# Performance work log

Hardware: AMD Instinct MI355X
Metric: run time of the kernel (lower is better)

Reference implementation:

```python
import jax, jax.numpy as jnp
import numpy as np

N_EMBD = 1024
N_HEAD = 16
B, T = 4, 2048


def setup_inputs() -> dict:
    key = jax.random.key(0)
    ks = jax.random.split(key, 4)
    s = 1.0 / np.sqrt(N_EMBD)
    return {
        "x": jax.random.normal(ks[0], (B, T, N_EMBD), dtype=jnp.float32),
        "w_attn": jax.random.normal(ks[1], (N_EMBD, 3 * N_EMBD), dtype=jnp.float32) * s,
        "b_attn": jnp.zeros((3 * N_EMBD,), dtype=jnp.float32),
        "w_proj": jax.random.normal(ks[2], (N_EMBD, N_EMBD), dtype=jnp.float32) * s,
        "b_proj": jnp.zeros((N_EMBD,), dtype=jnp.float32),
    }


def reference(x, w_attn, b_attn, w_proj, b_proj):
    Bb, Tt, C = x.shape
    H = N_HEAD
    D = C // H  # head dim
    qkv = x @ w_attn + b_attn  # [B,T,3C]
    q, k, v = jnp.split(qkv, 3, axis=2)
    # [B,H,T,D]
    q = q.reshape(Bb, Tt, H, D).transpose(0, 2, 1, 3)
    k = k.reshape(Bb, Tt, H, D).transpose(0, 2, 1, 3)
    v = v.reshape(Bb, Tt, H, D).transpose(0, 2, 1, 3)
    scale = 1.0 / np.sqrt(D).astype(np.float32)
    attn = jnp.einsum("bhqd,bhkd->bhqk", q, k) * scale
    mask = jnp.tril(jnp.ones((Tt, Tt), dtype=bool))
    attn = jnp.where(mask, attn, jnp.float32(-jnp.inf))
    probs = jax.nn.softmax(attn, axis=-1)
    out = jnp.einsum("bhqk,bhkd->bhqd", probs, v)
    out = out.transpose(0, 2, 1, 3).reshape(Bb, Tt, C)
    return out @ w_proj + b_proj
```

## Files before the change

### kernel.cpp

```cpp
#include <hip/hip_runtime.h>
#include <hip/hip_bf16.h>


typedef float f32x4 __attribute__((ext_vector_type(4)));
typedef float f32x16 __attribute__((ext_vector_type(16)));
typedef short short8 __attribute__((ext_vector_type(8)));
typedef short short4v __attribute__((ext_vector_type(4)));

__device__ __forceinline__ short f2bf(float f) {
  union { __hip_bfloat16 h; short s; } u;
  u.h = __float2bfloat16(f);
  return u.s;
}

__device__ __forceinline__ void gl_lds16(const void* g, void* l) {
  __builtin_amdgcn_global_load_lds(
      (const __attribute__((address_space(1))) void*)g,
      (__attribute__((address_space(3))) void*)l, 16, 0, 0);
}

__global__ void prep(const float* __restrict__ x, const float* __restrict__ wa,
                     const float* __restrict__ wp, short* __restrict__ xb,
                     short* __restrict__ wat, short* __restrict__ wpt) {
  const int bid = blockIdx.x, tid = threadIdx.x;
  if (bid < 8192) {
    int i = (bid * 256 + tid) * 4;
    float4 v = *(const float4*)(x + i);
    short4v o;
    o[0] = f2bf(v.x); o[1] = f2bf(v.y); o[2] = f2bf(v.z); o[3] = f2bf(v.w);
    *(short4v*)(xb + i) = o;
    return;
  }
  __shared__ float tile[32][33];
  const float* in;
  short* out;
  int N, bx, by;
  if (bid < 11264) {
    int t = bid - 8192;
    in = wa; out = wat; N = 3072; bx = t % 96; by = t / 96;
  } else {
    int t = bid - 11264;
    in = wp; out = wpt; N = 1024; bx = t & 31; by = t >> 5;
  }
  int tx = tid & 31, ty = tid >> 5;
  int x0 = bx * 32, y0 = by * 32;
#pragma unroll
  for (int i = 0; i < 32; i += 8)
    tile[ty + i][tx] = in[(size_t)(y0 + ty + i) * N + x0 + tx];
  __syncthreads();
#pragma unroll
  for (int i = 0; i < 32; i += 8)
    out[(size_t)(x0 + ty + i) * 1024 + y0 + tx] = f2bf(tile[tx][ty + i]);
}

#define GEMM_BODY(A_, Bt_)                                                        \
  __shared__ __align__(16) short As[2][128 * 32];                                 \
  __shared__ __align__(16) short Bs[2][128 * 32];                                 \
  const int tid = threadIdx.x;                                                    \
  const int wv = tid >> 6;                                                        \
  const int wr = wv >> 1, wc = wv & 1;                                            \
  const int col = tid & 31, khalf = (tid >> 5) & 1;                               \
  const int m0 = blockIdx.y * 128, n0 = blockIdx.x * 128;                         \
  const int cc0 = tid, cc1 = tid + 256;                                           \
  const int row0 = cc0 >> 2, part0 = ((cc0 & 3) - ((cc0 >> 3) & 3)) & 3;          \
  const int row1 = cc1 >> 2, part1 = ((cc1 & 3) - ((cc1 >> 3) & 3)) & 3;          \
  const size_t ga0 = (size_t)(m0 + row0) * 1024 + part0 * 8;                      \
  const size_t ga1 = (size_t)(m0 + row1) * 1024 + part1 * 8;                      \
  const size_t gb0 = (size_t)(n0 + row0) * 1024 + part0 * 8;                      \
  const size_t gb1 = (size_t)(n0 + row1) * 1024 + part1 * 8;                      \
  f32x16 acc[2][2];                                                               \
  _Pragma("unroll") for (int i = 0; i < 2; ++i)                                   \
      _Pragma("unroll") for (int j = 0; j < 2; ++j)                               \
          acc[i][j] = (f32x16)(0.f);                                              \
  gl_lds16(A_ + ga0, (char*)As[0] + cc0 * 16);                                    \
  gl_lds16(A_ + ga1, (char*)As[0] + cc1 * 16);                                    \
  gl_lds16(Bt_ + gb0, (char*)Bs[0] + cc0 * 16);                                   \
  gl_lds16(Bt_ + gb1, (char*)Bs[0] + cc1 * 16);                                   \
  __syncthreads();                                                                \
  for (int kt = 0; kt < 32; ++kt) {                                               \
    if (kt + 1 < 32) {                                                            \
      const int k0 = (kt + 1) * 32;                                               \
      char* Ad = (char*)As[(kt + 1) & 1];                                         \
      char* Bd = (char*)Bs[(kt + 1) & 1];                                         \
      gl_lds16(A_ + ga0 + k0, Ad + cc0 * 16);                                     \
      gl_lds16(A_ + ga1 + k0, Ad + cc1 * 16);                                     \
      gl_lds16(Bt_ + gb0 + k0, Bd + cc0 * 16);                                    \
      gl_lds16(Bt_ + gb1 + k0, Bd + cc1 * 16);                                    \
    }                                                                             \
    const short* Ac = As[kt & 1];                                                 \
    const short* Bc = Bs[kt & 1];                                                 \
    short8 af[2][2], bf[2][2];                                                    \
    _Pragma("unroll") for (int i = 0; i < 2; ++i)                                 \
        _Pragma("unroll") for (int s = 0; s < 2; ++s) {                           \
          int pa = s * 2 + khalf;                                                 \
          int ra = wr * 64 + i * 32 + col;                                        \
          int rb = wc * 64 + i * 32 + col;                                        \
          af[i][s] = *(const short8*)&Ac[(ra * 4 + ((pa + (ra >> 1)) & 3)) * 8];  \
          bf[i][s] = *(const short8*)&Bc[(rb * 4 + ((pa + (rb >> 1)) & 3)) * 8];  \
        }                                                                         \
    _Pragma("unroll") for (int s = 0; s < 2; ++s)                                 \
        _Pragma("unroll") for (int i = 0; i < 2; ++i)                             \
            _Pragma("unroll") for (int j = 0; j < 2; ++j)                         \
                acc[i][j] = __builtin_amdgcn_mfma_f32_32x32x16_bf16(              \
                    af[i][s], bf[j][s], acc[i][j], 0, 0, 0);                      \
    __syncthreads();                                                              \
  }

__global__ __launch_bounds__(256, 2) void gemm_qkv(
    const short* __restrict__ A, const short* __restrict__ Bt,
    const float* __restrict__ bias, short* __restrict__ Qb,
    short* __restrict__ Kb, short* __restrict__ Vtb) {
  GEMM_BODY(A, Bt)
  const int rhalf = khalf * 4;
#pragma unroll
  for (int i = 0; i < 2; ++i) {
#pragma unroll
    for (int j = 0; j < 2; ++j) {
      int n = n0 + wc * 64 + j * 32 + col;
      int n2 = n & 1023;
      int hh = n2 >> 6, d = n2 & 63;
      float bv = bias[n];
      int mb = m0 + wr * 64 + i * 32 + rhalf;
      int bb = mb >> 11;
      int bh = (bb << 4) + hh;
      if (n < 2048) {
        const bool isq = n < 1024;
#pragma unroll
        for (int a = 0; a < 16; ++a) {
          int t = (mb + (a & 3) + 8 * (a >> 2)) & 2047;
          float o = acc[i][j][a] + bv;
          size_t idx = ((size_t)bh * 2048 + t) * 64 + d;
          if (isq)
            Qb[idx] = f2bf(o * 0.18033688f);
          else
            Kb[idx] = f2bf(o);
        }
      } else {
        const int lnv = d & 15, mtv = d >> 4;
#pragma unroll
        for (int g = 0; g < 4; ++g) {
          int t0 = (mb + 8 * g) & 2047;
          int ktv = t0 >> 6, kbv = (t0 >> 4) & 3, qv = (t0 >> 2) & 3;
          short4v o;
#pragma unroll
          for (int r = 0; r < 4; ++r) o[r] = f2bf(acc[i][j][g * 4 + r] + bv);
          *(short4v*)&Vtb[(size_t)(((bh * 32 + ktv) * 4 + kbv) * 4 + mtv) * 256 +
                          (qv * 16 + lnv) * 4] = o;
        }
      }
    }
  }
}

__global__ __launch_bounds__(256, 2) void gemm_proj(
    const short* __restrict__ A, const short* __restrict__ Bt,
    const float* __restrict__ bias, float* __restrict__ out) {
  GEMM_BODY(A, Bt)
  const int rhalf = khalf * 4;
#pragma unroll
  for (int i = 0; i < 2; ++i) {
#pragma unroll
    for (int j = 0; j < 2; ++j) {
      int n = n0 + wc * 64 + j * 32 + col;
      float bv = bias[n];
      int mb = m0 + wr * 64 + i * 32 + rhalf;
#pragma unroll
      for (int a = 0; a < 16; ++a) {
        int m = mb + (a & 3) + 8 * (a >> 2);
        out[(size_t)m * 1024 + n] = acc[i][j][a] + bv;
      }
    }
  }
}

__global__ __launch_bounds__(256, 4) void flash_attn(
    const short* __restrict__ Qg_, const short* __restrict__ Kg_,
    const short* __restrict__ V4_, short* __restrict__ Ob) {
  const int tid = threadIdx.x;
  const int wv = tid >> 6, ln = tid & 15, quad = (tid & 63) >> 4;
  const int lane = tid & 63;
  const int bh = blockIdx.x & 63;
  const int g = blockIdx.x >> 6;
  const int c = g * 4 + wv;
  const int qbase = c * 32;
  const int nkt = ((qbase + 31) >> 6) + 1;
  const short* Qg = Qg_ + (size_t)bh * 2048 * 64;
  const short* Kg = Kg_ + (size_t)bh * 2048 * 64;
  const short* V4 = V4_ + (size_t)bh * 131072;
  const int bb = bh >> 4, hh = bh & 15;

  short8 qf[2][2];
#pragma unroll
  for (int h = 0; h < 2; ++h)
#pragma unroll
    for (int ch = 0; ch < 2; ++ch)
      qf[h][ch] = *(const short8*)(Qg + (size_t)(qbase + h * 16 + ln) * 64 +
                                   ch * 32 + quad * 8);

  f32x4 Oacc[2][4];
#pragma unroll
  for (int h = 0; h < 2; ++h)
#pragma unroll
    for (int mt = 0; mt < 4; ++mt) Oacc[h][mt] = (f32x4){0.f, 0.f, 0.f, 0.f};
  float lpart[2] = {0.f, 0.f};

  for (int kt = 0; kt < nkt; ++kt) {
    const short* Kt = Kg + (size_t)kt * 64 * 64;
    const short* Vt = V4 + (size_t)kt * 4096;

    f32x4 St[2][4];
#pragma unroll
    for (int h = 0; h < 2; ++h)
#pragma unroll
      for (int kb = 0; kb < 4; ++kb) St[h][kb] = (f32x4){0.f, 0.f, 0.f, 0.f};
    __builtin_amdgcn_s_setprio(1);
#pragma unroll
    for (int kb = 0; kb < 4; ++kb) {
      short8 ka0 = *(const short8*)(Kt + (size_t)(kb * 16 + ln) * 64 + quad * 8);
      short8 ka1 =
          *(const short8*)(Kt + (size_t)(kb * 16 + ln) * 64 + 32 + quad * 8);
#pragma unroll
      for (int h = 0; h < 2; ++h) {
        St[h][kb] = __builtin_amdgcn_mfma_f32_16x16x32_bf16(ka0, qf[h][0],
                                                            St[h][kb], 0, 0, 0);
        St[h][kb] = __builtin_amdgcn_mfma_f32_16x16x32_bf16(ka1, qf[h][1],
                                                            St[h][kb], 0, 0, 0);
      }
    }
    __builtin_amdgcn_s_setprio(0);

    short4v pf[2][4];
#pragma unroll
    for (int h = 0; h < 2; ++h) {
      float lp0 = 0.f, lp1 = 0.f;
      if (kt * 64 + 63 <= qbase + h * 16) {
#pragma unroll
        for (int kb = 0; kb < 4; ++kb) {
          float p[4];
#pragma unroll
          for (int r = 0; r < 4; ++r)
            p[r] = __builtin_amdgcn_exp2f(St[h][kb][r]);
          lp0 += p[0] + p[2];
          lp1 += p[1] + p[3];
          union { __hip_bfloat162 b2; unsigned u; } w0, w1;
          w0.b2 = __float22bfloat162_rn(make_float2(p[0], p[1]));
          w1.b2 = __float22bfloat162_rn(make_float2(p[2], p[3]));
          union { short4v s4; unsigned u2[2]; } m;
          m.u2[0] = w0.u; m.u2[1] = w1.u;
          pf[h][kb] = m.s4;
        }
      } else {
        const int qg = qbase + h * 16 + ln;
#pragma unroll
        for (int kb = 0; kb < 4; ++kb) {
          float p[4];
#pragma unroll
          for (int r = 0; r < 4; ++r) {
            int key = kt * 64 + kb * 16 + quad * 4 + r;
            float s = (key <= qg) ? St[h][kb][r] : -1e30f;
            p[r] = __builtin_amdgcn_exp2f(s);
          }
          lp0 += p[0] + p[2];
          lp1 += p[1] + p[3];
          union { __hip_bfloat162 b2; unsigned u; } w0, w1;
          w0.b2 = __float22bfloat162_rn(make_float2(p[0], p[1]));
          w1.b2 = __float22bfloat162_rn(make_float2(p[2], p[3]));
          union { short4v s4; unsigned u2[2]; } m;
          m.u2[0] = w0.u; m.u2[1] = w1.u;
          pf[h][kb] = m.s4;
        }
      }
      lpart[h] += lp0 + lp1;
    }

    __builtin_amdgcn_s_setprio(1);
#pragma unroll
    for (int kb = 0; kb < 4; ++kb)
#pragma unroll
      for (int mt = 0; mt < 4; ++mt) {
        short4v va =
            *(const short4v*)(Vt + (kb * 4 + mt) * 256 + lane * 4);
#pragma unroll
        for (int h = 0; h < 2; ++h)
          Oacc[h][mt] = __builtin_amdgcn_mfma_f32_16x16x16bf16_1k(
              va, pf[h][kb], Oacc[h][mt], 0, 0, 0);
      }
    __builtin_amdgcn_s_setprio(0);
  }

#pragma unroll
  for (int h = 0; h < 2; ++h) {
    float l = lpart[h];
    l += __shfl_xor(l, 16);
    l += __shfl_xor(l, 32);
    float rl = 1.0f / l;
    int t = qbase + h * 16 + ln;
#pragma unroll
    for (int mt = 0; mt < 4; ++mt) {
      short4v o;
#pragma unroll
      for (int r = 0; r < 4; ++r) o[r] = f2bf(Oacc[h][mt][r] * rl);
      *(short4v*)(Ob + ((size_t)(bb * 2048 + t)) * 1024 + hh * 64 + mt * 16 +
                  quad * 4) = o;
    }
  }
}


extern "C" void kernel_launch(void* const* d_in, const int* in_sizes, int n_in,
                              void* d_out, int out_size, void* d_ws, size_t ws_size,
                              hipStream_t stream) {
  const float* x      = (const float*)d_in[0];
  const float* w_attn = (const float*)d_in[1];
  const float* b_attn = (const float*)d_in[2];
  const float* w_proj = (const float*)d_in[3];
  const float* b_proj = (const float*)d_in[4];
  float* out = (float*)d_out;
  char* ws = (char*)d_ws;

  short* xb  = (short*)(ws);
  short* wat = (short*)(ws + 16777216);
  short* wpt = (short*)(ws + 23068672);
  short* Qb  = (short*)(ws + 25165824);
  short* Kb  = (short*)(ws + 41943040);
  short* Vtb = (short*)(ws + 58720256);
  short* Ob  = (short*)(ws + 75497472);

  prep<<<12288, 256, 0, stream>>>(x, w_attn, w_proj, xb, wat, wpt);
  gemm_qkv<<<dim3(24, 64), 256, 0, stream>>>(xb, wat, b_attn, Qb, Kb, Vtb);
  flash_attn<<<1024, 256, 0, stream>>>(Qb, Kb, Vtb, Ob);
  gemm_proj<<<dim3(8, 64), 256, 0, stream>>>(Ob, wpt, b_proj, out);
}
```

Baseline: 305.3 us.

## Rewrite QKV GEMM with 256x256 pipelined tiles and single-wave flash blocks

The QKV GEMM becomes a 512-thread kernel with 256x256 tiles, direct global-to-LDS loads, split-K double buffering and hand-placed waitcnt/barriers, so MFMA work overlaps with loads. Flash attention changes to one wave per block and schedules the longest causal rows first to balance load. It also double-buffers K fragments in registers and prefetches V ahead of the MFMAs. The manual waitcnt scheduling risks subtle ordering bugs and more register pressure.

```diff
diff --git a/kernel.cpp b/kernel.cpp
--- a/kernel.cpp
+++ b/kernel.cpp
@@ -106,21 +106,159 @@
     __syncthreads();                                                              \
   }
 
-__global__ __launch_bounds__(256, 2) void gemm_qkv(
+__global__ __launch_bounds__(256, 2) void gemm_proj(
+    const short* __restrict__ A, const short* __restrict__ Bt,
+    const float* __restrict__ bias, float* __restrict__ out) {
+  GEMM_BODY(A, Bt)
+  const int rhalf = khalf * 4;
+#pragma unroll
+  for (int i = 0; i < 2; ++i) {
+#pragma unroll
+    for (int j = 0; j < 2; ++j) {
+      int n = n0 + wc * 64 + j * 32 + col;
+      float bv = bias[n];
+      int mb = m0 + wr * 64 + i * 32 + rhalf;
+#pragma unroll
+      for (int a = 0; a < 16; ++a) {
+        int m = mb + (a & 3) + 8 * (a >> 2);
+        out[(size_t)m * 1024 + n] = acc[i][j][a] + bv;
+      }
+    }
+  }
+}
+
+#define BARRIER() asm volatile("s_barrier" ::: "memory")
+#define VMC(N) asm volatile("s_waitcnt vmcnt(" #N ")" ::: "memory")
+
+#define STG(KT, S, SRC, LB)                                                \
+  if ((KT) < 16) {                                                         \
+    char* db_ = (char*)(LB) + (((KT) & 1) ? 32768 : 0) + ((S) * 16384);    \
+    const short* sb_ = (SRC) + (KT) * 64 + (S) * 32;                       \
+    gl_lds16(sb_ + g_off0, db_ + d_off0);                                  \
+    gl_lds16(sb_ + g_off1, db_ + d_off1);                                  \
+  }
+
+#define LDF(AF, BF, ABP, BBP, S, AO, BO)                                   \
+  _Pragma("unroll") for (int mt_ = 0; mt_ < 4; ++mt_)                      \
+      AF[mt_] = *(const short8*)((ABP) + (S) * 16384 + (AO)[mt_]);         \
+  _Pragma("unroll") for (int nt_ = 0; nt_ < 2; ++nt_)                      \
+      BF[nt_] = *(const short8*)((BBP) + (S) * 16384 + (BO)[nt_]);
+
+#define MFMA8_BODY(AF, BF)                                                 \
+  __builtin_amdgcn_s_setprio(1);                                           \
+  _Pragma("unroll") for (int mt_ = 0; mt_ < 4; ++mt_)                      \
+      _Pragma("unroll") for (int nt_ = 0; nt_ < 2; ++nt_)                  \
+          acc[mt_][nt_] = __builtin_amdgcn_mfma_f32_32x32x16_bf16(         \
+              AF[mt_], BF[nt_], acc[mt_][nt_], 0, 0, 0);                   \
+  __builtin_amdgcn_s_setprio(0);
+
+#define MFMA8(AF, BF)                                                      \
+  __builtin_amdgcn_sched_barrier(0);                                       \
+  asm volatile("s_waitcnt lgkmcnt(6)" ::: "memory");                       \
+  MFMA8_BODY(AF, BF)
+
+#define MFMA8_LG0(AF, BF)                                                  \
+  __builtin_amdgcn_sched_barrier(0);                                       \
+  asm volatile("s_waitcnt lgkmcnt(0)" ::: "memory");                       \
+  MFMA8_BODY(AF, BF)
+
+__global__ __launch_bounds__(512, 2) void gemm_qkv(
     const short* __restrict__ A, const short* __restrict__ Bt,
     const float* __restrict__ bias, short* __restrict__ Qb,
     short* __restrict__ Kb, short* __restrict__ Vtb) {
-  GEMM_BODY(A, Bt)
+  __shared__ __align__(16) short Asm[2][16384];
+  __shared__ __align__(16) short Bsm[2][16384];
+  const int tid = threadIdx.x;
+  const int wv = tid >> 6;
+  const int wr = wv >> 2, wc = wv & 3;
+  const int ln32 = tid & 31, khalf = (tid >> 5) & 1;
+  const int m0 = blockIdx.y * 256, n0 = blockIdx.x * 256;
+
+  const int d_off0 = tid * 16, d_off1 = d_off0 + 8192;
+  const int pa_st = ((tid & 3) - ((tid >> 3) & 3)) & 3;
+  const size_t g_off0 = (size_t)(tid >> 2) * 1024 + (size_t)pa_st * 8;
+  const size_t g_off1 = g_off0 + (size_t)128 * 1024;
+
+  const int rot = (ln32 >> 1) & 3;
+  const int slotE = (khalf + rot) & 3;
+  const int slotO = (2 + khalf + rot) & 3;
+  int aoffE[4], aoffO[4], boffE[2], boffO[2];
+#pragma unroll
+  for (int mt = 0; mt < 4; ++mt) {
+    int r = (wr * 128 + mt * 32 + ln32) * 64;
+    aoffE[mt] = r + slotE * 16;
+    aoffO[mt] = r + slotO * 16;
+  }
+#pragma unroll
+  for (int nt = 0; nt < 2; ++nt) {
+    int r = (wc * 64 + nt * 32 + ln32) * 64;
+    boffE[nt] = r + slotE * 16;
+    boffO[nt] = r + slotO * 16;
+  }
+
+  const short* srcA = A + (size_t)m0 * 1024;
+  const short* srcB = Bt + (size_t)n0 * 1024;
+
+  f32x16 acc[4][2];
+#pragma unroll
+  for (int i = 0; i < 4; ++i)
+#pragma unroll
+    for (int j = 0; j < 2; ++j) acc[i][j] = (f32x16)(0.f);
+
+  short8 af0[4], af1[4], bf0[2], bf1[2];
+
+  STG(0, 0, srcA, Asm)
+  STG(0, 0, srcB, Bsm)
+  STG(0, 1, srcA, Asm)
+  STG(0, 1, srcB, Bsm)
+  STG(1, 0, srcA, Asm)
+  STG(1, 0, srcB, Bsm)
+  VMC(4);
+  BARRIER();
+  {
+    const char* Ab0 = (const char*)Asm;
+    const char* Bb0 = (const char*)Bsm;
+    LDF(af0, bf0, Ab0, Bb0, 0, aoffE, boffE)
+  }
+
+  for (int kt = 0; kt < 16; ++kt) {
+    const char* Ab = (const char*)Asm + ((kt & 1) << 15);
+    const char* Bb = (const char*)Bsm + ((kt & 1) << 15);
+    const char* An = (const char*)Asm + (((kt + 1) & 1) << 15);
+    const char* Bn = (const char*)Bsm + (((kt + 1) & 1) << 15);
+    LDF(af1, bf1, Ab, Bb, 0, aoffO, boffO)
+    STG(kt + 1, 1, srcA, Asm)
+    MFMA8(af0, bf0)
+    LDF(af0, bf0, Ab, Bb, 1, aoffE, boffE)
+    STG(kt + 1, 1, srcB, Bsm)
+    MFMA8(af1, bf1)
+    if (kt == 15) { VMC(0); } else { VMC(4); }
+    BARRIER();
+    LDF(af1, bf1, Ab, Bb, 1, aoffO, boffO)
+    STG(kt + 2, 0, srcA, Asm)
+    MFMA8(af0, bf0)
+    if (kt < 15) {
+      LDF(af0, bf0, An, Bn, 0, aoffE, boffE)
+      STG(kt + 2, 0, srcB, Bsm)
+      MFMA8(af1, bf1)
+      if (kt == 14) { VMC(0); } else { VMC(4); }
+    } else {
+      MFMA8_LG0(af1, bf1)
+    }
+    BARRIER();
+  }
+
+  const int col = tid & 31;
   const int rhalf = khalf * 4;
 #pragma unroll
-  for (int i = 0; i < 2; ++i) {
+  for (int i = 0; i < 4; ++i) {
 #pragma unroll
     for (int j = 0; j < 2; ++j) {
       int n = n0 + wc * 64 + j * 32 + col;
       int n2 = n & 1023;
       int hh = n2 >> 6, d = n2 & 63;
       float bv = bias[n];
-      int mb = m0 + wr * 64 + i * 32 + rhalf;
+      int mb = m0 + wr * 128 + i * 32 + rhalf;
       int bb = mb >> 11;
       int bh = (bb << 4) + hh;
       if (n < 2048) {
@@ -152,38 +290,94 @@
   }
 }
 
-__global__ __launch_bounds__(256, 2) void gemm_proj(
-    const short* __restrict__ A, const short* __restrict__ Bt,
-    const float* __restrict__ bias, float* __restrict__ out) {
-  GEMM_BODY(A, Bt)
-  const int rhalf = khalf * 4;
-#pragma unroll
-  for (int i = 0; i < 2; ++i) {
-#pragma unroll
-    for (int j = 0; j < 2; ++j) {
-      int n = n0 + wc * 64 + j * 32 + col;
-      float bv = bias[n];
-      int mb = m0 + wr * 64 + i * 32 + rhalf;
-#pragma unroll
-      for (int a = 0; a < 16; ++a) {
-        int m = mb + (a & 3) + 8 * (a >> 2);
-        out[(size_t)m * 1024 + n] = acc[i][j][a] + bv;
-      }
-    }
-  }
-}
-
-__global__ __launch_bounds__(256, 4) void flash_attn(
+
+#define LOADK(DST, KT)                                                        \
+  {                                                                           \
+    const short* Kt_ = Kg + (size_t)(KT) * 4096;                              \
+    _Pragma("unroll") for (int kb = 0; kb < 4; ++kb) {                        \
+      DST[kb][0] = *(const short8*)(Kt_ + (kb * 16 + ln) * 64 + quad * 8);    \
+      DST[kb][1] = *(const short8*)(Kt_ + (kb * 16 + ln) * 64 + 32 + quad * 8); \
+    }                                                                         \
+  }
+
+#define FCOMPUTE(KS, KT)                                                      \
+  {                                                                           \
+    const short* Vt_ = V4 + (size_t)(KT) * 4096;                              \
+    short4v vr[4][4];                                                         \
+    _Pragma("unroll") for (int kb = 0; kb < 4; ++kb)                          \
+        _Pragma("unroll") for (int mt = 0; mt < 4; ++mt)                      \
+            vr[kb][mt] =                                                      \
+                *(const short4v*)(Vt_ + (kb * 4 + mt) * 256 + lane * 4);      \
+    f32x4 St[2][4];                                                           \
+    _Pragma("unroll") for (int h = 0; h < 2; ++h)                             \
+        _Pragma("unroll") for (int kb = 0; kb < 4; ++kb)                      \
+            St[h][kb] = (f32x4){0.f, 0.f, 0.f, 0.f};                          \
+    __builtin_amdgcn_s_setprio(1);                                            \
+    _Pragma("unroll") for (int kb = 0; kb < 4; ++kb)                          \
+        _Pragma("unroll") for (int h = 0; h < 2; ++h) {                       \
+          St[h][kb] = __builtin_amdgcn_mfma_f32_16x16x32_bf16(                \
+              KS[kb][0], qf[h][0], St[h][kb], 0, 0, 0);                       \
+          St[h][kb] = __builtin_amdgcn_mfma_f32_16x16x32_bf16(                \
+              KS[kb][1], qf[h][1], St[h][kb], 0, 0, 0);                       \
+        }                                                                     \
+    __builtin_amdgcn_s_setprio(0);                                            \
+    short4v pf[2][4];                                                         \
+    _Pragma("unroll") for (int h = 0; h < 2; ++h) {                           \
+      float lp0 = 0.f, lp1 = 0.f;                                             \
+      if ((KT)*64 + 63 <= qbase + h * 16) {                                   \
+        _Pragma("unroll") for (int kb = 0; kb < 4; ++kb) {                    \
+          float p[4];                                                         \
+          _Pragma("unroll") for (int r = 0; r < 4; ++r)                       \
+              p[r] = __builtin_amdgcn_exp2f(St[h][kb][r]);                    \
+          lp0 += p[0] + p[2];                                                 \
+          lp1 += p[1] + p[3];                                                 \
+          union { __hip_bfloat162 b2; unsigned u; } w0, w1;                   \
+          w0.b2 = __float22bfloat162_rn(make_float2(p[0], p[1]));             \
+          w1.b2 = __float22bfloat162_rn(make_float2(p[2], p[3]));             \
+          union { short4v s4; unsigned u2[2]; } mm;                           \
+          mm.u2[0] = w0.u; mm.u2[1] = w1.u;                                   \
+          pf[h][kb] = mm.s4;                                                  \
+        }                                                                     \
+      } else {                                                                \
+        const int qg = qbase + h * 16 + ln;                                   \
+        _Pragma("unroll") for (int kb = 0; kb < 4; ++kb) {                    \
+          float p[4];                                                         \
+          _Pragma("unroll") for (int r = 0; r < 4; ++r) {                     \
+            int key = (KT)*64 + kb * 16 + quad * 4 + r;                       \
+            float s = (key <= qg) ? St[h][kb][r] : -1e30f;                    \
+            p[r] = __builtin_amdgcn_exp2f(s);                                 \
+          }                                                                   \
+          lp0 += p[0] + p[2];                                                 \
+          lp1 += p[1] + p[3];                                                 \
+          union { __hip_bfloat162 b2; unsigned u; } w0, w1;                   \
+          w0.b2 = __float22bfloat162_rn(make_float2(p[0], p[1]));             \
+          w1.b2 = __float22bfloat162_rn(make_float2(p[2], p[3]));             \
+          union { short4v s4; unsigned u2[2]; } mm;                           \
+          mm.u2[0] = w0.u; mm.u2[1] = w1.u;                                   \
+          pf[h][kb] = mm.s4;                                                  \
+        }                                                                     \
+      }                                                                       \
+      lpart[h] += lp0 + lp1;                                                  \
+    }                                                                         \
+    __builtin_amdgcn_s_setprio(1);                                            \
+    _Pragma("unroll") for (int kb = 0; kb < 4; ++kb)                          \
+        _Pragma("unroll") for (int mt = 0; mt < 4; ++mt)                      \
+            _Pragma("unroll") for (int h = 0; h < 2; ++h)                     \
+                Oacc[h][mt] = __builtin_amdgcn_mfma_f32_16x16x16bf16_1k(      \
+                    vr[kb][mt], pf[h][kb], Oacc[h][mt], 0, 0, 0);             \
+    __builtin_amdgcn_s_setprio(0);                                            \
+  }
+
+__global__ __launch_bounds__(64, 4) void flash_attn(
     const short* __restrict__ Qg_, const short* __restrict__ Kg_,
     const short* __restrict__ V4_, short* __restrict__ Ob) {
   const int tid = threadIdx.x;
-  const int wv = tid >> 6, ln = tid & 15, quad = (tid & 63) >> 4;
-  const int lane = tid & 63;
+  const int ln = tid & 15, quad = (tid >> 4) & 3;
+  const int lane = tid;
   const int bh = blockIdx.x & 63;
-  const int g = blockIdx.x >> 6;
-  const int c = g * 4 + wv;
+  const int c = 63 - (blockIdx.x >> 6);
   const int qbase = c * 32;
-  const int nkt = ((qbase + 31) >> 6) + 1;
+  const int nkt = (c >> 1) + 1;
   const short* Qg = Qg_ + (size_t)bh * 2048 * 64;
   const short* Kg = Kg_ + (size_t)bh * 2048 * 64;
   const short* V4 = V4_ + (size_t)bh * 131072;
@@ -204,88 +398,18 @@
     for (int mt = 0; mt < 4; ++mt) Oacc[h][mt] = (f32x4){0.f, 0.f, 0.f, 0.f};
   float lpart[2] = {0.f, 0.f};
 
-  for (int kt = 0; kt < nkt; ++kt) {
-    const short* Kt = Kg + (size_t)kt * 64 * 64;
-    const short* Vt = V4 + (size_t)kt * 4096;
-
-    f32x4 St[2][4];
-#pragma unroll
-    for (int h = 0; h < 2; ++h)
-#pragma unroll
-      for (int kb = 0; kb < 4; ++kb) St[h][kb] = (f32x4){0.f, 0.f, 0.f, 0.f};
-    __builtin_amdgcn_s_setprio(1);
-#pragma unroll
-    for (int kb = 0; kb < 4; ++kb) {
-      short8 ka0 = *(const short8*)(Kt + (size_t)(kb * 16 + ln) * 64 + quad * 8);
-      short8 ka1 =
-          *(const short8*)(Kt + (size_t)(kb * 16 + ln) * 64 + 32 + quad * 8);
-#pragma unroll
-      for (int h = 0; h < 2; ++h) {
-        St[h][kb] = __builtin_amdgcn_mfma_f32_16x16x32_bf16(ka0, qf[h][0],
-                                                            St[h][kb], 0, 0, 0);
-        St[h][kb] = __builtin_amdgcn_mfma_f32_16x16x32_bf16(ka1, qf[h][1],
-                                                            St[h][kb], 0, 0, 0);
-      }
-    }
-    __builtin_amdgcn_s_setprio(0);
-
-    short4v pf[2][4];
-#pragma unroll
-    for (int h = 0; h < 2; ++h) {
-      float lp0 = 0.f, lp1 = 0.f;
-      if (kt * 64 + 63 <= qbase + h * 16) {
-#pragma unroll
-        for (int kb = 0; kb < 4; ++kb) {
-          float p[4];
-#pragma unroll
-          for (int r = 0; r < 4; ++r)
-            p[r] = __builtin_amdgcn_exp2f(St[h][kb][r]);
-          lp0 += p[0] + p[2];
-          lp1 += p[1] + p[3];
-          union { __hip_bfloat162 b2; unsigned u; } w0, w1;
-          w0.b2 = __float22bfloat162_rn(make_float2(p[0], p[1]));
-          w1.b2 = __float22bfloat162_rn(make_float2(p[2], p[3]));
-          union { short4v s4; unsigned u2[2]; } m;
-          m.u2[0] = w0.u; m.u2[1] = w1.u;
-          pf[h][kb] = m.s4;
-        }
-      } else {
-        const int qg = qbase + h * 16 + ln;
-#pragma unroll
-        for (int kb = 0; kb < 4; ++kb) {
-          float p[4];
-#pragma unroll
-          for (int r = 0; r < 4; ++r) {
-            int key = kt * 64 + kb * 16 + quad * 4 + r;
-            float s = (key <= qg) ? St[h][kb][r] : -1e30f;
-            p[r] = __builtin_amdgcn_exp2f(s);
-          }
-          lp0 += p[0] + p[2];
-          lp1 += p[1] + p[3];
-          union { __hip_bfloat162 b2; unsigned u; } w0, w1;
-          w0.b2 = __float22bfloat162_rn(make_float2(p[0], p[1]));
-          w1.b2 = __float22bfloat162_rn(make_float2(p[2], p[3]));
-          union { short4v s4; unsigned u2[2]; } m;
-          m.u2[0] = w0.u; m.u2[1] = w1.u;
-          pf[h][kb] = m.s4;
-        }
-      }
-      lpart[h] += lp0 + lp1;
-    }
-
-    __builtin_amdgcn_s_setprio(1);
-#pragma unroll
-    for (int kb = 0; kb < 4; ++kb)
-#pragma unroll
-      for (int mt = 0; mt < 4; ++mt) {
-        short4v va =
-            *(const short4v*)(Vt + (kb * 4 + mt) * 256 + lane * 4);
-#pragma unroll
-        for (int h = 0; h < 2; ++h)
-          Oacc[h][mt] = __builtin_amdgcn_mfma_f32_16x16x16bf16_1k(
-              va, pf[h][kb], Oacc[h][mt], 0, 0, 0);
-      }
-    __builtin_amdgcn_s_setprio(0);
+  short8 kA[4][2], kB[4][2];
+  LOADK(kA, 0)
+  int kt = 0;
+  while (true) {
+    if (kt + 1 < nkt) LOADK(kB, kt + 1)
+    FCOMPUTE(kA, kt)
+    ++kt;
+    if (kt == nkt) break;
+    if (kt + 1 < nkt) LOADK(kA, kt + 1)
+    FCOMPUTE(kB, kt)
+    ++kt;
+    if (kt == nkt) break;
   }
 
 #pragma unroll
@@ -327,7 +451,7 @@
   short* Ob  = (short*)(ws + 75497472);
 
   prep<<<12288, 256, 0, stream>>>(x, w_attn, w_proj, xb, wat, wpt);
-  gemm_qkv<<<dim3(24, 64), 256, 0, stream>>>(xb, wat, b_attn, Qb, Kb, Vtb);
-  flash_attn<<<1024, 256, 0, stream>>>(Qb, Kb, Vtb, Ob);
+  gemm_qkv<<<dim3(12, 32), 512, 0, stream>>>(xb, wat, b_attn, Qb, Kb, Vtb);
+  flash_attn<<<4096, 64, 0, stream>>>(Qb, Kb, Vtb, Ob);
   gemm_proj<<<dim3(8, 64), 256, 0, stream>>>(Ob, wpt, b_proj, out);
 }
```

After: 523.3 us. +71.4%, slower.
